# Kernel optimization log

Measured on AMD Instinct MI355X. Metric: run time of the kernel, lower is better.

Reference implementation:

```python
import jax, jax.numpy as jnp
import numpy as np

N_NODES = 50000
N_EDGES = 800000
IN_DIM = 64
EDGE_DIM = 16
HID = 128
L = 3
G = 128  # number of graphs in the batch
EPS = 1e-5


def _glorot(key, shape):
    fan_in, fan_out = shape[0], shape[1]
    lim = float(np.sqrt(6.0 / (fan_in + fan_out)))
    return jax.random.uniform(key, shape, jnp.float32, -lim, lim)


def setup_inputs() -> dict:
    key = jax.random.key(0)
    ks = jax.random.split(key, 40)
    inp = {}
    inp["x"] = jax.random.uniform(ks[0], (N_NODES, IN_DIM), jnp.float32)
    inp["edge_index"] = jax.random.randint(ks[1], (2, N_EDGES), 0, N_NODES, jnp.int64)
    inp["edge_attr"] = jax.random.normal(ks[2], (N_EDGES, EDGE_DIM), jnp.float32)
    inp["batch"] = jnp.sort(jax.random.randint(ks[3], (N_NODES,), 0, G, jnp.int64))
    # ligand / protein input MLPs: Linear-ReLU-Linear-ReLU
    inp["lig_w1"] = _glorot(ks[4], (IN_DIM, HID)); inp["lig_b1"] = jnp.zeros((HID,), jnp.float32)
    inp["lig_w2"] = _glorot(ks[5], (HID, HID));    inp["lig_b2"] = jnp.zeros((HID,), jnp.float32)
    inp["prot_w1"] = _glorot(ks[6], (IN_DIM, HID)); inp["prot_b1"] = jnp.zeros((HID,), jnp.float32)
    inp["prot_w2"] = _glorot(ks[7], (HID, HID));    inp["prot_b2"] = jnp.zeros((HID,), jnp.float32)
    # per-layer GINEConv params (stacked over layers)
    inp["edge_w"] = jnp.stack([_glorot(ks[8 + i], (EDGE_DIM, HID)) for i in range(L)])
    inp["edge_b"] = jnp.zeros((L, HID), jnp.float32)
    inp["nn_w1"] = jnp.stack([_glorot(ks[12 + i], (HID, HID)) for i in range(L)])
    inp["nn_b1"] = jnp.zeros((L, HID), jnp.float32)
    inp["nn_w2"] = jnp.stack([_glorot(ks[16 + i], (HID, HID)) for i in range(L)])
    inp["nn_b2"] = jnp.zeros((L, HID), jnp.float32)
    # GraphNorm params: weight=1, bias=0, mean_scale=1
    inp["gn_w"] = jnp.ones((L, HID), jnp.float32)
    inp["gn_b"] = jnp.zeros((L, HID), jnp.float32)
    inp["gn_ms"] = jnp.ones((L, HID), jnp.float32)
    # output head: Linear-ReLU-Linear(1)
    inp["fc_w1"] = _glorot(ks[20], (HID, HID)); inp["fc_b1"] = jnp.zeros((HID,), jnp.float32)
    inp["fc_w2"] = _glorot(ks[21], (HID, 1));   inp["fc_b2"] = jnp.zeros((1,), jnp.float32)
    return inp


def reference(x, edge_index, edge_attr, batch,
              lig_w1, lig_b1, lig_w2, lig_b2,
              prot_w1, prot_b1, prot_w2, prot_b2,
              edge_w, edge_b, nn_w1, nn_b1, nn_w2, nn_b2,
              gn_w, gn_b, gn_ms,
              fc_w1, fc_b1, fc_w2, fc_b2):
    relu = lambda a: jnp.maximum(a, 0)
    src, dst = edge_index[0], edge_index[1]

    # input encoders, merged per node by protein flag (last feature column)
    is_prot = x[:, -1] > 0.5
    h_lig = relu(relu(x @ lig_w1 + lig_b1) @ lig_w2 + lig_b2)
    h_prot = relu(relu(x @ prot_w1 + prot_b1) @ prot_w2 + prot_b2)
    h = jnp.where(is_prot[:, None], h_prot, h_lig)

    # per-graph node counts for GraphNorm
    cnt = jax.ops.segment_sum(jnp.ones((x.shape[0],), jnp.float32), batch, num_segments=G)
    cnt = jnp.maximum(cnt, 1.0)[:, None]

    for l in range(L):
        # GINEConv (eps=0): out = nn(x + sum_{j->i} relu(x_j + lin(e_ji)))
        e = edge_attr @ edge_w[l] + edge_b[l]              # [E, HID]
        msg = relu(h[src] + e)                             # gather + add + relu
        aggr = jax.ops.segment_sum(msg, dst, num_segments=h.shape[0])
        h = aggr + h
        h = relu(h @ nn_w1[l] + nn_b1[l]) @ nn_w2[l] + nn_b2[l]
        # GraphNorm: per-graph mean/var with learnable mean_scale
        mean = jax.ops.segment_sum(h, batch, num_segments=G) / cnt
        hc = h - mean[batch] * gn_ms[l]
        var = jax.ops.segment_sum(hc * hc, batch, num_segments=G) / cnt
        h = gn_w[l] * hc * jax.lax.rsqrt(var[batch] + EPS) + gn_b[l]
        h = relu(h)  # (dropout=0.0 -> identity)

    g = jax.ops.segment_sum(h, batch, num_segments=G)      # global_add_pool
    out = relu(g @ fc_w1 + fc_b1) @ fc_w2 + fc_b2
    return out.reshape(-1)
```

## Files before the change

### kernel.cpp

```cpp
#include <hip/hip_runtime.h>

#define N_NODES 50000
#define N_EDGES 800000
#define IN_DIM  64
#define EDGE_DIM 16
#define HID     128
#define NLAYERS 3
#define NGRAPH  128
#define EPS     1e-5f

#define BSHIFT  7
#define NB      391
#define BCAP    4064

typedef __attribute__((ext_vector_type(8))) short bf8_t;
typedef __attribute__((ext_vector_type(4))) short bf4_t;
typedef __attribute__((ext_vector_type(4))) float f32x4;

__device__ __forceinline__ unsigned short f2bf(float x) {
    unsigned u = __float_as_uint(x);
    unsigned r = u + 0x7fffu + ((u >> 16) & 1u);
    return (unsigned short)(r >> 16);
}
__device__ __forceinline__ float bf2f(unsigned short v) {
    return __uint_as_float(((unsigned)v) << 16);
}

__global__ void k_init(int* __restrict__ bcnt_pad, float* __restrict__ pool,
                       float* __restrict__ gsum, float* __restrict__ gsq) {
    int i = blockIdx.x * blockDim.x + threadIdx.x;
    if (i < NB * 16) bcnt_pad[i] = 0;
    if (i < NGRAPH * HID) pool[i] = 0.0f;
    if (i < NLAYERS * NGRAPH * HID) { gsum[i] = 0.0f; gsq[i] = 0.0f; }
}

__global__ __launch_bounds__(NGRAPH) void k_count(const int* __restrict__ batch,
                                                  float* __restrict__ cnt) {
    int g = threadIdx.x;
    int lo = 0, hi = N_NODES;
    while (lo < hi) { int mid = (lo + hi) >> 1; if (batch[mid] < g) lo = mid + 1; else hi = mid; }
    int a = lo;
    lo = 0; hi = N_NODES;
    while (lo < hi) { int mid = (lo + hi) >> 1; if (batch[mid] < g + 1) lo = mid + 1; else hi = mid; }
    cnt[g] = (float)(lo - a);
}

__global__ void k_wconv(const float* __restrict__ nw1, const float* __restrict__ nw2,
                        unsigned short* __restrict__ wt) {
    int idx = blockIdx.x * 256 + threadIdx.x;
    if (idx >= NLAYERS * 2 * HID * HID) return;
    int k = idx & 127;
    int n = (idx >> 7) & 127;
    int which = (idx >> 14) & 1;
    int l = idx >> 15;
    const float* w = (which == 0 ? nw1 : nw2) + l * HID * HID;
    wt[idx] = f2bf(w[k * HID + n]);
}

__global__ void k_wconv_enc(const float* __restrict__ lw1, const float* __restrict__ pw1,
                            const float* __restrict__ lw2, const float* __restrict__ pw2,
                            unsigned short* __restrict__ we) {
    int idx = blockIdx.x * 256 + threadIdx.x;
    if (idx >= 49152) return;
    float v;
    if (idx < 8192)       { int n = idx >> 6, k = idx & 63;            v = lw1[k * HID + n]; }
    else if (idx < 16384) { int r = idx - 8192;  int n = r >> 6, k = r & 63;  v = pw1[k * HID + n]; }
    else if (idx < 32768) { int r = idx - 16384; int n = r >> 7, k = r & 127; v = lw2[k * HID + n]; }
    else                  { int r = idx - 32768; int n = r >> 7, k = r & 127; v = pw2[k * HID + n]; }
    we[idx] = f2bf(v);
}

__global__ void k_wconv_e(const float* __restrict__ ew, const float* __restrict__ eb,
                          unsigned short* __restrict__ wte) {
    int idx = blockIdx.x * 256 + threadIdx.x;
    if (idx >= NLAYERS * 8 * 64 * 8) return;
    int j = idx & 7;
    int lane = (idx >> 3) & 63;
    int t = (idx >> 9) & 7;
    int l = idx >> 12;
    int k = (lane >> 4) * 8 + j;
    int feat = t * 16 + (lane & 15);
    float v = 0.0f;
    if (k < EDGE_DIM)       v = ew[l * EDGE_DIM * HID + k * HID + feat];
    else if (k == EDGE_DIM) v = eb[l * HID + feat];
    wte[idx] = f2bf(v);
}

__global__ void k_bfill(const int* __restrict__ srcs, const int* __restrict__ dsts,
                        int* __restrict__ bcnt_pad, int2* __restrict__ bkt) {
    int e = blockIdx.x * blockDim.x + threadIdx.x;
    if (e < N_EDGES) {
        int d = dsts[e];
        int b = d >> BSHIFT;
        int pos = atomicAdd(&bcnt_pad[b * 16], 1);
        if (pos < BCAP)
            bkt[(size_t)b * BCAP + pos] = make_int2(srcs[e], ((d & 127) << 20) | e);
    }
}

__global__ __launch_bounds__(512) void k_bscan(const int* __restrict__ bcnt_pad,
                                               int* __restrict__ boff) {
    __shared__ int s[512];
    int t = threadIdx.x;
    int v = (t < NB) ? bcnt_pad[t * 16] : 0;
    s[t] = v; __syncthreads();
    for (int off = 1; off < 512; off <<= 1) {
        int x = (t >= off) ? s[t - off] : 0;
        __syncthreads();
        s[t] += x;
        __syncthreads();
    }
    if (t < NB) boff[t] = s[t] - v;
    if (t == NB - 1) boff[NB] = s[t];
}

__global__ __launch_bounds__(256) void k_bcsr(const int* __restrict__ bcnt_pad,
                                              const int* __restrict__ boff,
                                              const int2* __restrict__ bkt,
                                              int* __restrict__ row_start,
                                              int* __restrict__ row_end,
                                              int2* __restrict__ csr_se) {
    __shared__ int lcnt[128];
    __shared__ int lsc[128];
    __shared__ int lfill[128];
    int b = blockIdx.x, t = threadIdx.x;
    int base = boff[b];
    int ecnt = bcnt_pad[b * 16]; if (ecnt > BCAP) ecnt = BCAP;
    if (t < 128) lcnt[t] = 0;
    __syncthreads();
    for (int i = t; i < ecnt; i += 256) {
        int2 en = bkt[(size_t)b * BCAP + i];
        atomicAdd(&lcnt[(en.y >> 20) & 127], 1);
    }
    __syncthreads();
    if (t < 128) lsc[t] = lcnt[t];
    __syncthreads();
    for (int off = 1; off < 128; off <<= 1) {
        int x = (t < 128 && t >= off) ? lsc[t - off] : 0;
        __syncthreads();
        if (t < 128) lsc[t] += x;
        __syncthreads();
    }
    if (t < 128) {
        int excl = lsc[t] - lcnt[t];
        lfill[t] = excl;
        int node = (b << BSHIFT) + t;
        if (node < N_NODES) {
            row_start[node] = base + excl;
            row_end[node]   = base + excl + lcnt[t];
        }
    }
    __syncthreads();
    for (int i = t; i < ecnt; i += 256) {
        int2 en = bkt[(size_t)b * BCAP + i];
        int q = atomicAdd(&lfill[(en.y >> 20) & 127], 1);
        csr_se[base + q] = make_int2(en.x, en.y & 0xFFFFF);
    }
}

__global__ __launch_bounds__(256) void k_reorder(const int2* __restrict__ csr_se,
                                                 const float* __restrict__ ea,
                                                 int* __restrict__ csr_src,
                                                 unsigned short* __restrict__ cea) {
    int p = blockIdx.x * blockDim.x + threadIdx.x;
    if (p < N_EDGES) {
        int2 se = csr_se[p];
        csr_src[p] = se.x;
        const float* s = ea + (size_t)se.y * EDGE_DIM;
        float4 a0 = *(const float4*)(s);
        float4 a1 = *(const float4*)(s + 4);
        float4 a2 = *(const float4*)(s + 8);
        float4 a3 = *(const float4*)(s + 12);
        bf8_t v0, v1;
        v0[0] = (short)f2bf(a0.x); v0[1] = (short)f2bf(a0.y);
        v0[2] = (short)f2bf(a0.z); v0[3] = (short)f2bf(a0.w);
        v0[4] = (short)f2bf(a1.x); v0[5] = (short)f2bf(a1.y);
        v0[6] = (short)f2bf(a1.z); v0[7] = (short)f2bf(a1.w);
        v1[0] = (short)f2bf(a2.x); v1[1] = (short)f2bf(a2.y);
        v1[2] = (short)f2bf(a2.z); v1[3] = (short)f2bf(a2.w);
        v1[4] = (short)f2bf(a3.x); v1[5] = (short)f2bf(a3.y);
        v1[6] = (short)f2bf(a3.z); v1[7] = (short)f2bf(a3.w);
        *(bf8_t*)(cea + (size_t)p * EDGE_DIM) = v0;
        *(bf8_t*)(cea + (size_t)p * EDGE_DIM + 8) = v1;
    }
}

#define HS 136
__global__ __launch_bounds__(256, 8) void k_encoder_mfma(
    const float* __restrict__ x,
    const unsigned short* __restrict__ we,
    const float* __restrict__ lb1, const float* __restrict__ lb2,
    const float* __restrict__ pb1, const float* __restrict__ pb2,
    unsigned short* __restrict__ Hbp) {
    __shared__ short h1s[4][16 * HS];
    int w = threadIdx.x >> 6, lane = threadIdx.x & 63;
    int m = lane & 15, quad = lane >> 4;
    int tile = w >> 1, role = w & 1;
    int nb = blockIdx.x * 32 + tile * 16;
    short* hl = h1s[w];
    int nclamp = nb + m; if (nclamp >= N_NODES) nclamp = N_NODES - 1;
    const float* xp = x + (size_t)nclamp * IN_DIM;
    const float* b1 = role ? pb1 : lb1;
    const float* b2 = role ? pb2 : lb2;
    const unsigned short* w1 = we + role * 8192;
    const unsigned short* w2 = we + 16384 + role * 16384;

    f32x4 a1[8];
    #pragma unroll
    for (int t = 0; t < 8; ++t) {
        float bv = b1[t * 16 + m];
        a1[t] = (f32x4){bv, bv, bv, bv};
    }
    #pragma unroll
    for (int s_ = 0; s_ < 2; ++s_) {
        int k0 = s_ * 32 + quad * 8;
        float4 a0 = *(const float4*)(xp + k0);
        float4 a1v = *(const float4*)(xp + k0 + 4);
        bf8_t af;
        af[0] = (short)f2bf(a0.x); af[1] = (short)f2bf(a0.y);
        af[2] = (short)f2bf(a0.z); af[3] = (short)f2bf(a0.w);
        af[4] = (short)f2bf(a1v.x); af[5] = (short)f2bf(a1v.y);
        af[6] = (short)f2bf(a1v.z); af[7] = (short)f2bf(a1v.w);
        #pragma unroll
        for (int t = 0; t < 8; ++t) {
            bf8_t bw = *(const bf8_t*)(w1 + (t * 16 + m) * 64 + k0);
            a1[t] = __builtin_amdgcn_mfma_f32_16x16x32_bf16(af, bw, a1[t], 0, 0, 0);
        }
    }
    #pragma unroll
    for (int t = 0; t < 8; ++t)
        #pragma unroll
        for (int r = 0; r < 4; ++r)
            hl[(quad * 4 + r) * HS + t * 16 + m] = (short)f2bf(fmaxf(a1[t][r], 0.0f));
    __syncthreads();
    f32x4 a2[8];
    #pragma unroll
    for (int t = 0; t < 8; ++t) {
        float bv = b2[t * 16 + m];
        a2[t] = (f32x4){bv, bv, bv, bv};
    }
    #pragma unroll
    for (int s_ = 0; s_ < 4; ++s_) {
        int k0 = s_ * 32 + quad * 8;
        bf8_t af = *(const bf8_t*)(hl + m * HS + k0);
        #pragma unroll
        for (int t = 0; t < 8; ++t) {
            bf8_t bw = *(const bf8_t*)(w2 + (t * 16 + m) * 128 + k0);
            a2[t] = __builtin_amdgcn_mfma_f32_16x16x32_bf16(af, bw, a2[t], 0, 0, 0);
        }
    }
    #pragma unroll
    for (int r = 0; r < 4; ++r) {
        int node = nb + quad * 4 + r;
        if (node < N_NODES) {
            bool prot = x[(size_t)node * IN_DIM + (IN_DIM - 1)] > 0.5f;
            if (prot == (role == 1)) {
                bf8_t o;
                #pragma unroll
                for (int t = 0; t < 8; ++t)
                    o[t] = (short)f2bf(fmaxf(a2[t][r], 0.0f));
                *(bf8_t*)(Hbp + (size_t)node * HID + m * 8) = o;
            }
        }
    }
}

__global__ __launch_bounds__(256, 8) void k_gather(
    const int* __restrict__ csr_src, const unsigned short* __restrict__ cea,
    const int* __restrict__ row_start, const int* __restrict__ row_end,
    const unsigned short* __restrict__ wte,
    const unsigned short* __restrict__ Hbp, unsigned short* __restrict__ Abp) {
    int w = threadIdx.x >> 6, lane = threadIdx.x & 63;
    int m = lane & 15, quad = lane >> 4;
    int n = blockIdx.x * 2 + (w >> 1);
    int half = w & 1;

    bf8_t bw[4];
    #pragma unroll
    for (int t = 0; t < 4; ++t)
        bw[t] = *(const bf8_t*)(wte + ((size_t)(half * 4 + t) * 64 + lane) * 8);

    float acc[4];
    #pragma unroll
    for (int t = 0; t < 4; ++t) acc[t] = 0.0f;

    int p  = __builtin_amdgcn_readfirstlane(row_start[n]);
    int pe = __builtin_amdgcn_readfirstlane(row_end[n]);

    const f32x4 zc = (f32x4){0.0f, 0.0f, 0.0f, 0.0f};

    for (; p + 16 <= pe; p += 16) {
        bf8_t af = (bf8_t){0, 0, 0, 0, 0, 0, 0, 0};
        if (quad < 2)
            af = *(const bf8_t*)(cea + (size_t)(p + m) * EDGE_DIM + quad * 8);
        else if (quad == 2)
            af[0] = (short)0x3F80;
        int sr[4];
        #pragma unroll
        for (int r = 0; r < 4; ++r) sr[r] = csr_src[p + quad * 4 + r];
        bf4_t hrow[4];
        #pragma unroll
        for (int r = 0; r < 4; ++r)
            hrow[r] = *(const bf4_t*)(Hbp + (size_t)sr[r] * HID + m * 8 + half * 4);
        f32x4 d[4];
        #pragma unroll
        for (int t = 0; t < 4; ++t)
            d[t] = __builtin_amdgcn_mfma_f32_16x16x32_bf16(af, bw[t], zc, 0, 0, 0);
        #pragma unroll
        for (int t = 0; t < 4; ++t)
            #pragma unroll
            for (int r = 0; r < 4; ++r)
                acc[t] += fmaxf(bf2f((unsigned short)hrow[r][t]) + d[t][r], 0.0f);
    }
    int rem = pe - p;
    if (rem > 0) {
        bf8_t af = (bf8_t){0, 0, 0, 0, 0, 0, 0, 0};
        if (quad < 2 && m < rem)
            af = *(const bf8_t*)(cea + (size_t)(p + m) * EDGE_DIM + quad * 8);
        else if (quad == 2)
            af[0] = (short)0x3F80;
        int sr[4];
        #pragma unroll
        for (int r = 0; r < 4; ++r) {
            int idx = p + quad * 4 + r; if (idx >= pe) idx = pe - 1;
            sr[r] = csr_src[idx];
        }
        bf4_t hrow[4];
        #pragma unroll
        for (int r = 0; r < 4; ++r)
            hrow[r] = *(const bf4_t*)(Hbp + (size_t)sr[r] * HID + m * 8 + half * 4);
        f32x4 d[4];
        #pragma unroll
        for (int t = 0; t < 4; ++t)
            d[t] = __builtin_amdgcn_mfma_f32_16x16x32_bf16(af, bw[t], zc, 0, 0, 0);
        #pragma unroll
        for (int t = 0; t < 4; ++t)
            #pragma unroll
            for (int r = 0; r < 4; ++r)
                if (quad * 4 + r < rem)
                    acc[t] += fmaxf(bf2f((unsigned short)hrow[r][t]) + d[t][r], 0.0f);
    }
    #pragma unroll
    for (int t = 0; t < 4; ++t) {
        acc[t] += __shfl_xor(acc[t], 16);
        acc[t] += __shfl_xor(acc[t], 32);
    }
    float asel = (quad == 0) ? acc[0] : (quad == 1) ? acc[1] : (quad == 2) ? acc[2] : acc[3];
    float self_ = bf2f(Hbp[(size_t)n * HID + m * 8 + half * 4 + quad]);
    Abp[(size_t)n * HID + (half * 4 + quad) * 16 + m] = f2bf(asel + self_);
}

#define MLP_NODES_PER_BLOCK 32
__global__ __launch_bounds__(256, 6) void k_mlp_mfma(
    const unsigned short* __restrict__ Abp, const int* __restrict__ batch,
    const unsigned short* __restrict__ wt1, const unsigned short* __restrict__ wt2,
    const float* __restrict__ b1, const float* __restrict__ b2,
    unsigned short* __restrict__ Hb, float* __restrict__ gsum, float* __restrict__ gsq) {
    __shared__ short h1s[2][16 * HS];
    int w = threadIdx.x >> 6;
    int lane = threadIdx.x & 63;
    int m = lane & 15;
    int quad = lane >> 4;
    int tile = w >> 1, role = w & 1;
    int nb = blockIdx.x * MLP_NODES_PER_BLOCK + tile * 16;
    short* hw = h1s[tile];
    int fbase = role * 64;

    int nclamp = nb + m; if (nclamp >= N_NODES) nclamp = N_NODES - 1;
    const unsigned short* Ap = Abp + (size_t)nclamp * HID;
    f32x4 acc1[4];
    #pragma unroll
    for (int t = 0; t < 4; ++t) {
        float bv = b1[fbase + t * 16 + m];
        acc1[t] = (f32x4){bv, bv, bv, bv};
    }
    #pragma unroll
    for (int s_ = 0; s_ < 4; ++s_) {
        int k0 = s_ * 32 + quad * 8;
        bf8_t af = *(const bf8_t*)(Ap + k0);
        #pragma unroll
        for (int t = 0; t < 4; ++t) {
            bf8_t bf = *(const bf8_t*)(wt1 + (size_t)(fbase + t * 16 + m) * HID + k0);
            acc1[t] = __builtin_amdgcn_mfma_f32_16x16x32_bf16(af, bf, acc1[t], 0, 0, 0);
        }
    }
    #pragma unroll
    for (int t = 0; t < 4; ++t)
        #pragma unroll
        for (int r = 0; r < 4; ++r) {
            float v = fmaxf(acc1[t][r], 0.0f);
            hw[(quad * 4 + r) * HS + fbase + t * 16 + m] = (short)f2bf(v);
        }
    __syncthreads();
    f32x4 acc2[4];
    #pragma unroll
    for (int t = 0; t < 4; ++t) {
        float bv = b2[fbase + t * 16 + m];
        acc2[t] = (f32x4){bv, bv, bv, bv};
    }
    #pragma unroll
    for (int s_ = 0; s_ < 4; ++s_) {
        int k0 = s_ * 32 + quad * 8;
        bf8_t af = *(const bf8_t*)(hw + m * HS + k0);
        #pragma unroll
        for (int t = 0; t < 4; ++t) {
            bf8_t bf = *(const bf8_t*)(wt2 + (size_t)(fbase + t * 16 + m) * HID + k0);
            acc2[t] = __builtin_amdgcn_mfma_f32_16x16x32_bf16(af, bf, acc2[t], 0, 0, 0);
        }
    }
    #pragma unroll
    for (int t = 0; t < 4; ++t)
        #pragma unroll
        for (int r = 0; r < 4; ++r) {
            int node = nb + quad * 4 + r;
            if (node < N_NODES) Hb[(size_t)node * HID + fbase + t * 16 + m] = f2bf(acc2[t][r]);
        }
    int blast = nb + 15 < N_NODES ? batch[nb + 15] : -1;
    int g0 = batch[nb < N_NODES ? nb : N_NODES - 1];
    if (nb + 15 < N_NODES && g0 == blast) {
        #pragma unroll
        for (int t = 0; t < 4; ++t) {
            float s = 0.0f, q = 0.0f;
            #pragma unroll
            for (int r = 0; r < 4; ++r) { float v = acc2[t][r]; s += v; q += v * v; }
            s += __shfl_xor(s, 16); q += __shfl_xor(q, 16);
            s += __shfl_xor(s, 32); q += __shfl_xor(q, 32);
            if (quad == 0) {
                atomicAdd(&gsum[g0 * HID + fbase + t * 16 + m], s);
                atomicAdd(&gsq[g0 * HID + fbase + t * 16 + m], q);
            }
        }
    } else {
        #pragma unroll
        for (int t = 0; t < 4; ++t)
            #pragma unroll
            for (int r = 0; r < 4; ++r) {
                int node = nb + quad * 4 + r;
                if (node < N_NODES) {
                    int g = batch[node];
                    float v = acc2[t][r];
                    atomicAdd(&gsum[g * HID + fbase + t * 16 + m], v);
                    atomicAdd(&gsq[g * HID + fbase + t * 16 + m], v * v);
                }
            }
    }
}

#define NORM_N 8
__global__ __launch_bounds__(HID) void k_norm(
    const unsigned short* __restrict__ Hb, const int* __restrict__ batch,
    const float* __restrict__ gsum, const float* __restrict__ gsq,
    const float* __restrict__ cnt,
    const float* __restrict__ gw, const float* __restrict__ gb,
    const float* __restrict__ gms,
    unsigned short* __restrict__ Hbp, float* __restrict__ pool, int accumulate) {
    int n0 = blockIdx.x * NORM_N;
    int t = threadIdx.x;
    int m = t & 15, tt = t >> 4;
    float ms = gms[t], gwt = gw[t], gbt = gb[t];
    int g0 = batch[n0], gN = batch[n0 + NORM_N - 1];
    if (g0 == gN) {
        float c = fmaxf(cnt[g0], 1.0f);
        float mean = gsum[g0 * HID + t] / c;
        float msq  = gsq[g0 * HID + t] / c;
        float var = fmaxf(msq - mean * mean * ms * (2.0f - ms), 0.0f);
        float ssc = gwt * rsqrtf(var + EPS);
        float sof = gbt - ssc * mean * ms;
        float ps = 0.0f;
        #pragma unroll
        for (int i = 0; i < NORM_N; ++i) {
            float v = fmaxf(bf2f(Hb[(size_t)(n0 + i) * HID + t]) * ssc + sof, 0.0f);
            Hbp[(size_t)(n0 + i) * HID + m * 8 + tt] = f2bf(v);
            ps += v;
        }
        if (accumulate) atomicAdd(&pool[g0 * HID + t], ps);
    } else {
        #pragma unroll
        for (int i = 0; i < NORM_N; ++i) {
            int g = batch[n0 + i];
            float c = fmaxf(cnt[g], 1.0f);
            float mean = gsum[g * HID + t] / c;
            float msq  = gsq[g * HID + t] / c;
            float var = fmaxf(msq - mean * mean * ms * (2.0f - ms), 0.0f);
            float ssc = gwt * rsqrtf(var + EPS);
            float sof = gbt - ssc * mean * ms;
            float v = fmaxf(bf2f(Hb[(size_t)(n0 + i) * HID + t]) * ssc + sof, 0.0f);
            Hbp[(size_t)(n0 + i) * HID + m * 8 + tt] = f2bf(v);
            if (accumulate) atomicAdd(&pool[g * HID + t], v);
        }
    }
}

__global__ __launch_bounds__(HID) void k_head(
    const float* __restrict__ pool,
    const float* __restrict__ fw1, const float* __restrict__ fb1,
    const float* __restrict__ fw2, const float* __restrict__ fb2,
    float* __restrict__ out) {
    __shared__ float ps[HID];
    __shared__ float red[2];
    int g = blockIdx.x;
    int t = threadIdx.x;
    ps[t] = pool[g * HID + t];
    __syncthreads();
    float acc = fb1[t];
    #pragma unroll 4
    for (int k = 0; k < HID; ++k) acc = fmaf(ps[k], fw1[k * HID + t], acc);
    float p = fmaxf(acc, 0.0f) * fw2[t];
    #pragma unroll
    for (int off = 32; off > 0; off >>= 1) p += __shfl_down(p, off, 64);
    if ((t & 63) == 0) red[t >> 6] = p;
    __syncthreads();
    if (t == 0) out[g] = red[0] + red[1] + fb2[0];
}

extern "C" void kernel_launch(void* const* d_in, const int* in_sizes, int n_in,
                              void* d_out, int out_size, void* d_ws, size_t ws_size,
                              hipStream_t stream) {
    const float* x     = (const float*)d_in[0];
    const int*   ei    = (const int*)d_in[1];
    const float* ea    = (const float*)d_in[2];
    const int*   batch = (const int*)d_in[3];
    const float* lw1 = (const float*)d_in[4];
    const float* lb1 = (const float*)d_in[5];
    const float* lw2 = (const float*)d_in[6];
    const float* lb2 = (const float*)d_in[7];
    const float* pw1 = (const float*)d_in[8];
    const float* pb1 = (const float*)d_in[9];
    const float* pw2 = (const float*)d_in[10];
    const float* pb2 = (const float*)d_in[11];
    const float* ew  = (const float*)d_in[12];
    const float* eb  = (const float*)d_in[13];
    const float* nw1 = (const float*)d_in[14];
    const float* nb1 = (const float*)d_in[15];
    const float* nw2 = (const float*)d_in[16];
    const float* nb2 = (const float*)d_in[17];
    const float* gw  = (const float*)d_in[18];
    const float* gb  = (const float*)d_in[19];
    const float* gms = (const float*)d_in[20];
    const float* fw1 = (const float*)d_in[21];
    const float* fb1 = (const float*)d_in[22];
    const float* fw2 = (const float*)d_in[23];
    const float* fb2 = (const float*)d_in[24];
    float* out = (float*)d_out;

    float* ws   = (float*)d_ws;
    float* H    = ws;
    float* A    = H    + (size_t)N_NODES * HID;
    float* gsum = A    + (size_t)N_NODES * HID;
    float* gsq  = gsum + NLAYERS * NGRAPH * HID;
    float* pool = gsq  + NLAYERS * NGRAPH * HID;
    float* cnt  = pool + NGRAPH * HID;
    int* bcnt_pad  = (int*)(cnt + NGRAPH);
    int* boff      = bcnt_pad + NB * 16;
    int* row_start = boff + 512;
    int* row_end   = row_start + N_NODES;
    int* csr_src   = row_end + N_NODES;
    unsigned short* cea  = (unsigned short*)(csr_src + N_EDGES);
    unsigned short* wt   = cea + (size_t)N_EDGES * EDGE_DIM;
    unsigned short* wenc = wt + NLAYERS * 2 * HID * HID;
    unsigned short* wte  = wenc + 49152;
    unsigned short* Hbp  = wte + NLAYERS * 8 * 64 * 8;
    unsigned short* Hb   = (unsigned short*)H;
    unsigned short* Abp  = (unsigned short*)A;
    int2* bkt    = (int2*)(Abp + (size_t)N_NODES * HID);
    int2* csr_se = (int2*)H;

    const int* srcs = ei;
    const int* dsts = ei + N_EDGES;

    k_init<<<(N_NODES + 255) / 256, 256, 0, stream>>>(bcnt_pad, pool, gsum, gsq);
    k_count<<<1, NGRAPH, 0, stream>>>(batch, cnt);
    k_wconv<<<(NLAYERS * 2 * HID * HID + 255) / 256, 256, 0, stream>>>(nw1, nw2, wt);
    k_wconv_enc<<<(49152 + 255) / 256, 256, 0, stream>>>(lw1, pw1, lw2, pw2, wenc);
    k_wconv_e<<<(NLAYERS * 8 * 64 * 8 + 255) / 256, 256, 0, stream>>>(ew, eb, wte);
    k_bfill<<<(N_EDGES + 255) / 256, 256, 0, stream>>>(srcs, dsts, bcnt_pad, bkt);
    k_bscan<<<1, 512, 0, stream>>>(bcnt_pad, boff);
    k_bcsr<<<NB, 256, 0, stream>>>(bcnt_pad, boff, bkt, row_start, row_end, csr_se);
    k_reorder<<<(N_EDGES + 255) / 256, 256, 0, stream>>>(csr_se, ea, csr_src, cea);

    k_encoder_mfma<<<(N_NODES + 31) / 32, 256, 0, stream>>>(
        x, wenc, lb1, lb2, pb1, pb2, Hbp);

    int mlp_blocks = (N_NODES + MLP_NODES_PER_BLOCK - 1) / MLP_NODES_PER_BLOCK;
    for (int l = 0; l < NLAYERS; ++l) {
        k_gather<<<N_NODES / 2, 256, 0, stream>>>(
            csr_src, cea, row_start, row_end,
            wte + (size_t)l * 4096, Hbp, Abp);
        k_mlp_mfma<<<mlp_blocks, 256, 0, stream>>>(
            Abp, batch,
            wt + (size_t)l * 2 * HID * HID,
            wt + (size_t)l * 2 * HID * HID + HID * HID,
            nb1 + l * HID, nb2 + l * HID,
            Hb, gsum + (size_t)l * NGRAPH * HID, gsq + (size_t)l * NGRAPH * HID);
        k_norm<<<N_NODES / NORM_N, HID, 0, stream>>>(
            Hb, batch,
            gsum + (size_t)l * NGRAPH * HID, gsq + (size_t)l * NGRAPH * HID,
            cnt, gw + l * HID, gb + l * HID, gms + l * HID,
            Hbp, pool, (l == NLAYERS - 1) ? 1 : 0);
    }
    k_head<<<NGRAPH, HID, 0, stream>>>(pool, fw1, fb1, fw2, fb2, out);
}
```

Measured before the change: 618.2 us.

## Merge setup kernels, fuse reorder into CSR build, vectorize GraphNorm kernel

Folds the graph-count kernel into the init kernel and the three weight-conversion kernels into one, which cuts launch count. The CSR build kernel now writes the source indices and bf16 edge attributes directly, dropping the intermediate csr_se buffer and the separate reorder pass. The norm kernel is rewritten to handle 16 nodes per 256-thread block with 8-wide bf16 vector loads and stores. It stages the permuted output through shared memory and reduces the pooled sums in shared memory before issuing global atomics. The fused CSR pass now does scattered edge-attribute reads inside atomic-ordered loops, and the shared-memory atomics add contention.

```diff
diff --git a/kernel.cpp b/kernel.cpp
--- a/kernel.cpp
+++ b/kernel.cpp
@@ -27,63 +27,59 @@
 }
 
 __global__ void k_init(int* __restrict__ bcnt_pad, float* __restrict__ pool,
-                       float* __restrict__ gsum, float* __restrict__ gsq) {
+                       float* __restrict__ gsum, float* __restrict__ gsq,
+                       const int* __restrict__ batch, float* __restrict__ cnt) {
     int i = blockIdx.x * blockDim.x + threadIdx.x;
     if (i < NB * 16) bcnt_pad[i] = 0;
     if (i < NGRAPH * HID) pool[i] = 0.0f;
     if (i < NLAYERS * NGRAPH * HID) { gsum[i] = 0.0f; gsq[i] = 0.0f; }
-}
-
-__global__ __launch_bounds__(NGRAPH) void k_count(const int* __restrict__ batch,
-                                                  float* __restrict__ cnt) {
-    int g = threadIdx.x;
-    int lo = 0, hi = N_NODES;
-    while (lo < hi) { int mid = (lo + hi) >> 1; if (batch[mid] < g) lo = mid + 1; else hi = mid; }
-    int a = lo;
-    lo = 0; hi = N_NODES;
-    while (lo < hi) { int mid = (lo + hi) >> 1; if (batch[mid] < g + 1) lo = mid + 1; else hi = mid; }
-    cnt[g] = (float)(lo - a);
-}
-
-__global__ void k_wconv(const float* __restrict__ nw1, const float* __restrict__ nw2,
-                        unsigned short* __restrict__ wt) {
+    if (blockIdx.x == 0 && threadIdx.x < NGRAPH) {
+        int g = threadIdx.x;
+        int lo = 0, hi = N_NODES;
+        while (lo < hi) { int mid = (lo + hi) >> 1; if (batch[mid] < g) lo = mid + 1; else hi = mid; }
+        int a = lo;
+        lo = 0; hi = N_NODES;
+        while (lo < hi) { int mid = (lo + hi) >> 1; if (batch[mid] < g + 1) lo = mid + 1; else hi = mid; }
+        cnt[g] = (float)(lo - a);
+    }
+}
+
+__global__ void k_wall(const float* __restrict__ nw1, const float* __restrict__ nw2,
+                       const float* __restrict__ lw1, const float* __restrict__ pw1,
+                       const float* __restrict__ lw2, const float* __restrict__ pw2,
+                       const float* __restrict__ ew, const float* __restrict__ eb,
+                       unsigned short* __restrict__ wt,
+                       unsigned short* __restrict__ we,
+                       unsigned short* __restrict__ wte) {
     int idx = blockIdx.x * 256 + threadIdx.x;
-    if (idx >= NLAYERS * 2 * HID * HID) return;
-    int k = idx & 127;
-    int n = (idx >> 7) & 127;
-    int which = (idx >> 14) & 1;
-    int l = idx >> 15;
-    const float* w = (which == 0 ? nw1 : nw2) + l * HID * HID;
-    wt[idx] = f2bf(w[k * HID + n]);
-}
-
-__global__ void k_wconv_enc(const float* __restrict__ lw1, const float* __restrict__ pw1,
-                            const float* __restrict__ lw2, const float* __restrict__ pw2,
-                            unsigned short* __restrict__ we) {
-    int idx = blockIdx.x * 256 + threadIdx.x;
-    if (idx >= 49152) return;
-    float v;
-    if (idx < 8192)       { int n = idx >> 6, k = idx & 63;            v = lw1[k * HID + n]; }
-    else if (idx < 16384) { int r = idx - 8192;  int n = r >> 6, k = r & 63;  v = pw1[k * HID + n]; }
-    else if (idx < 32768) { int r = idx - 16384; int n = r >> 7, k = r & 127; v = lw2[k * HID + n]; }
-    else                  { int r = idx - 32768; int n = r >> 7, k = r & 127; v = pw2[k * HID + n]; }
-    we[idx] = f2bf(v);
-}
-
-__global__ void k_wconv_e(const float* __restrict__ ew, const float* __restrict__ eb,
-                          unsigned short* __restrict__ wte) {
-    int idx = blockIdx.x * 256 + threadIdx.x;
-    if (idx >= NLAYERS * 8 * 64 * 8) return;
-    int j = idx & 7;
-    int lane = (idx >> 3) & 63;
-    int t = (idx >> 9) & 7;
-    int l = idx >> 12;
-    int k = (lane >> 4) * 8 + j;
-    int feat = t * 16 + (lane & 15);
-    float v = 0.0f;
-    if (k < EDGE_DIM)       v = ew[l * EDGE_DIM * HID + k * HID + feat];
-    else if (k == EDGE_DIM) v = eb[l * HID + feat];
-    wte[idx] = f2bf(v);
+    if (idx < 98304) {
+        int k = idx & 127;
+        int n = (idx >> 7) & 127;
+        int which = (idx >> 14) & 1;
+        int l = idx >> 15;
+        const float* w = (which == 0 ? nw1 : nw2) + l * HID * HID;
+        wt[idx] = f2bf(w[k * HID + n]);
+    } else if (idx < 147456) {
+        int r0 = idx - 98304;
+        float v;
+        if (r0 < 8192)       { int n = r0 >> 6, k = r0 & 63;            v = lw1[k * HID + n]; }
+        else if (r0 < 16384) { int r = r0 - 8192;  int n = r >> 6, k = r & 63;  v = pw1[k * HID + n]; }
+        else if (r0 < 32768) { int r = r0 - 16384; int n = r >> 7, k = r & 127; v = lw2[k * HID + n]; }
+        else                 { int r = r0 - 32768; int n = r >> 7, k = r & 127; v = pw2[k * HID + n]; }
+        we[r0] = f2bf(v);
+    } else if (idx < 159744) {
+        int r0 = idx - 147456;
+        int j = r0 & 7;
+        int lane = (r0 >> 3) & 63;
+        int t = (r0 >> 9) & 7;
+        int l = r0 >> 12;
+        int k = (lane >> 4) * 8 + j;
+        int feat = t * 16 + (lane & 15);
+        float v = 0.0f;
+        if (k < EDGE_DIM)       v = ew[l * EDGE_DIM * HID + k * HID + feat];
+        else if (k == EDGE_DIM) v = eb[l * HID + feat];
+        wte[r0] = f2bf(v);
+    }
 }
 
 __global__ void k_bfill(const int* __restrict__ srcs, const int* __restrict__ dsts,
@@ -117,9 +113,11 @@
 __global__ __launch_bounds__(256) void k_bcsr(const int* __restrict__ bcnt_pad,
                                               const int* __restrict__ boff,
                                               const int2* __restrict__ bkt,
+                                              const float* __restrict__ ea,
                                               int* __restrict__ row_start,
                                               int* __restrict__ row_end,
-                                              int2* __restrict__ csr_se) {
+                                              int* __restrict__ csr_src,
+                                              unsigned short* __restrict__ cea) {
     __shared__ int lcnt[128];
     __shared__ int lsc[128];
     __shared__ int lfill[128];
@@ -154,19 +152,10 @@
     for (int i = t; i < ecnt; i += 256) {
         int2 en = bkt[(size_t)b * BCAP + i];
         int q = atomicAdd(&lfill[(en.y >> 20) & 127], 1);
-        csr_se[base + q] = make_int2(en.x, en.y & 0xFFFFF);
-    }
-}
-
-__global__ __launch_bounds__(256) void k_reorder(const int2* __restrict__ csr_se,
-                                                 const float* __restrict__ ea,
-                                                 int* __restrict__ csr_src,
-                                                 unsigned short* __restrict__ cea) {
-    int p = blockIdx.x * blockDim.x + threadIdx.x;
-    if (p < N_EDGES) {
-        int2 se = csr_se[p];
-        csr_src[p] = se.x;
-        const float* s = ea + (size_t)se.y * EDGE_DIM;
+        int p = base + q;
+        csr_src[p] = en.x;
+        int eid = en.y & 0xFFFFF;
+        const float* s = ea + (size_t)eid * EDGE_DIM;
         float4 a0 = *(const float4*)(s);
         float4 a1 = *(const float4*)(s + 4);
         float4 a2 = *(const float4*)(s + 8);
@@ -446,48 +435,65 @@
     }
 }
 
-#define NORM_N 8
-__global__ __launch_bounds__(HID) void k_norm(
+#define NORM_N 16
+__global__ __launch_bounds__(256) void k_norm(
     const unsigned short* __restrict__ Hb, const int* __restrict__ batch,
     const float* __restrict__ gsum, const float* __restrict__ gsq,
     const float* __restrict__ cnt,
     const float* __restrict__ gw, const float* __restrict__ gb,
     const float* __restrict__ gms,
     unsigned short* __restrict__ Hbp, float* __restrict__ pool, int accumulate) {
+    __shared__ float ssc[HID];
+    __shared__ float sof[HID];
+    __shared__ float lp[HID];
+    __shared__ short rp[NORM_N][HID];
     int n0 = blockIdx.x * NORM_N;
     int t = threadIdx.x;
-    int m = t & 15, tt = t >> 4;
-    float ms = gms[t], gwt = gw[t], gbt = gb[t];
+    int nl = t >> 4, c = t & 15;
+    int n = n0 + nl;
     int g0 = batch[n0], gN = batch[n0 + NORM_N - 1];
     if (g0 == gN) {
-        float c = fmaxf(cnt[g0], 1.0f);
-        float mean = gsum[g0 * HID + t] / c;
-        float msq  = gsq[g0 * HID + t] / c;
-        float var = fmaxf(msq - mean * mean * ms * (2.0f - ms), 0.0f);
-        float ssc = gwt * rsqrtf(var + EPS);
-        float sof = gbt - ssc * mean * ms;
-        float ps = 0.0f;
-        #pragma unroll
-        for (int i = 0; i < NORM_N; ++i) {
-            float v = fmaxf(bf2f(Hb[(size_t)(n0 + i) * HID + t]) * ssc + sof, 0.0f);
-            Hbp[(size_t)(n0 + i) * HID + m * 8 + tt] = f2bf(v);
-            ps += v;
-        }
-        if (accumulate) atomicAdd(&pool[g0 * HID + t], ps);
+        if (t < HID) {
+            float cg = fmaxf(cnt[g0], 1.0f);
+            float mean = gsum[g0 * HID + t] / cg;
+            float msq  = gsq[g0 * HID + t] / cg;
+            float ms = gms[t];
+            float var = fmaxf(msq - mean * mean * ms * (2.0f - ms), 0.0f);
+            float s = gw[t] * rsqrtf(var + EPS);
+            ssc[t] = s;
+            sof[t] = gb[t] - s * mean * ms;
+            lp[t] = 0.0f;
+        }
+        __syncthreads();
+        bf8_t hv = *(const bf8_t*)(Hb + (size_t)n * HID + c * 8);
+        #pragma unroll
+        for (int j = 0; j < 8; ++j) {
+            int f = c * 8 + j;
+            float v = fmaxf(bf2f((unsigned short)hv[j]) * ssc[f] + sof[f], 0.0f);
+            rp[nl][(f & 15) * 8 + (f >> 4)] = (short)f2bf(v);
+            if (accumulate) atomicAdd(&lp[f], v);
+        }
+        __syncthreads();
+        *(bf8_t*)(Hbp + (size_t)n * HID + c * 8) = *(bf8_t*)&rp[nl][c * 8];
+        if (accumulate && t < HID) atomicAdd(&pool[g0 * HID + t], lp[t]);
     } else {
-        #pragma unroll
-        for (int i = 0; i < NORM_N; ++i) {
-            int g = batch[n0 + i];
-            float c = fmaxf(cnt[g], 1.0f);
-            float mean = gsum[g * HID + t] / c;
-            float msq  = gsq[g * HID + t] / c;
+        int g = batch[n];
+        float cg = fmaxf(cnt[g], 1.0f);
+        bf8_t hv = *(const bf8_t*)(Hb + (size_t)n * HID + c * 8);
+        #pragma unroll
+        for (int j = 0; j < 8; ++j) {
+            int f = c * 8 + j;
+            float mean = gsum[g * HID + f] / cg;
+            float msq  = gsq[g * HID + f] / cg;
+            float ms = gms[f];
             float var = fmaxf(msq - mean * mean * ms * (2.0f - ms), 0.0f);
-            float ssc = gwt * rsqrtf(var + EPS);
-            float sof = gbt - ssc * mean * ms;
-            float v = fmaxf(bf2f(Hb[(size_t)(n0 + i) * HID + t]) * ssc + sof, 0.0f);
-            Hbp[(size_t)(n0 + i) * HID + m * 8 + tt] = f2bf(v);
-            if (accumulate) atomicAdd(&pool[g * HID + t], v);
-        }
+            float s = gw[f] * rsqrtf(var + EPS);
+            float v = fmaxf(bf2f((unsigned short)hv[j]) * s + (gb[f] - s * mean * ms), 0.0f);
+            rp[nl][(f & 15) * 8 + (f >> 4)] = (short)f2bf(v);
+            if (accumulate) atomicAdd(&pool[g * HID + f], v);
+        }
+        __syncthreads();
+        *(bf8_t*)(Hbp + (size_t)n * HID + c * 8) = *(bf8_t*)&rp[nl][c * 8];
     }
 }
 
@@ -563,20 +569,18 @@
     unsigned short* Hb   = (unsigned short*)H;
     unsigned short* Abp  = (unsigned short*)A;
     int2* bkt    = (int2*)(Abp + (size_t)N_NODES * HID);
-    int2* csr_se = (int2*)H;
 
     const int* srcs = ei;
     const int* dsts = ei + N_EDGES;
 
-    k_init<<<(N_NODES + 255) / 256, 256, 0, stream>>>(bcnt_pad, pool, gsum, gsq);
-    k_count<<<1, NGRAPH, 0, stream>>>(batch, cnt);
-    k_wconv<<<(NLAYERS * 2 * HID * HID + 255) / 256, 256, 0, stream>>>(nw1, nw2, wt);
-    k_wconv_enc<<<(49152 + 255) / 256, 256, 0, stream>>>(lw1, pw1, lw2, pw2, wenc);
-    k_wconv_e<<<(NLAYERS * 8 * 64 * 8 + 255) / 256, 256, 0, stream>>>(ew, eb, wte);
+    k_init<<<(NLAYERS * NGRAPH * HID + 255) / 256, 256, 0, stream>>>(
+        bcnt_pad, pool, gsum, gsq, batch, cnt);
+    k_wall<<<(159744 + 255) / 256, 256, 0, stream>>>(
+        nw1, nw2, lw1, pw1, lw2, pw2, ew, eb, wt, wenc, wte);
     k_bfill<<<(N_EDGES + 255) / 256, 256, 0, stream>>>(srcs, dsts, bcnt_pad, bkt);
     k_bscan<<<1, 512, 0, stream>>>(bcnt_pad, boff);
-    k_bcsr<<<NB, 256, 0, stream>>>(bcnt_pad, boff, bkt, row_start, row_end, csr_se);
-    k_reorder<<<(N_EDGES + 255) / 256, 256, 0, stream>>>(csr_se, ea, csr_src, cea);
+    k_bcsr<<<NB, 256, 0, stream>>>(bcnt_pad, boff, bkt, ea,
+                                   row_start, row_end, csr_src, cea);
 
     k_encoder_mfma<<<(N_NODES + 31) / 32, 256, 0, stream>>>(
         x, wenc, lb1, lb2, pb1, pb2, Hbp);
@@ -592,7 +596,7 @@
             wt + (size_t)l * 2 * HID * HID + HID * HID,
             nb1 + l * HID, nb2 + l * HID,
             Hb, gsum + (size_t)l * NGRAPH * HID, gsq + (size_t)l * NGRAPH * HID);
-        k_norm<<<N_NODES / NORM_N, HID, 0, stream>>>(
+        k_norm<<<N_NODES / NORM_N, 256, 0, stream>>>(
             Hb, batch,
             gsum + (size_t)l * NGRAPH * HID, gsq + (size_t)l * NGRAPH * HID,
             cnt, gw + l * HID, gb + l * HID, gms + l * HID,
```

After: 655.7 us. 6.1% more time.
